# Kernel optimization log

Measured on AMD Instinct MI355X. Metric: run time of the kernel, lower is better.

## Reference

```python
import jax, jax.numpy as jnp
import numpy as np

M_DIM, Z_DIM, C = 256, 128, 32
N, L = 512, 384


def setup_inputs() -> dict:
    key = jax.random.key(0)
    ks = jax.random.split(key, 9)
    s = 1.0 / np.sqrt(M_DIM)
    return {
        "m": jax.random.normal(ks[0], (N, L, M_DIM), dtype=jnp.float32),
        "ln_gamma": jnp.ones((M_DIM,), jnp.float32),
        "ln_beta": jnp.zeros((M_DIM,), jnp.float32),
        "w1": jax.random.normal(ks[1], (M_DIM, C), jnp.float32) * s,
        "b1": jnp.zeros((C,), jnp.float32),
        "w2": jax.random.normal(ks[2], (M_DIM, C), jnp.float32) * s,
        "b2": jnp.zeros((C,), jnp.float32),
        "w3": jax.random.normal(ks[3], (C * C, Z_DIM), jnp.float32) * (1.0 / np.sqrt(C * C)),
        "b3": jnp.zeros((Z_DIM,), jnp.float32),
    }


def _layernorm(x, gamma, beta, eps=1e-5):
    mu = jnp.mean(x, axis=-1, keepdims=True)
    var = jnp.mean(jnp.square(x - mu), axis=-1, keepdims=True)
    return (x - mu) * jax.lax.rsqrt(var + eps) * gamma + beta


def reference(m, ln_gamma, ln_beta, w1, b1, w2, b2, w3, b3):
    n = m.shape[0]
    o = _layernorm(m, ln_gamma, ln_beta)          # (N, L, D)
    a = o @ w2 + b2                                # (N, L, C)  linear2
    b = o @ w1 + b1                                # (N, L, C)  linear1
    # mean over N of outer products: reassociated as a single contraction over n
    op = jnp.einsum('nia,njb->ijab', a, b) / n     # (L, L, C, C)
    ll = op.shape[0]
    z = op.reshape(ll, ll, -1) @ w3 + b3           # (L, L, Z)
    return z
```

## Files before the change

kernel.cpp:

```cpp
#include <hip/hip_runtime.h>
#include <hip/hip_bf16.h>
#include <stdint.h>

#define L_DIM 384
#define MD    256
#define CC    32
#define ZD    128
#define NB    512
#define K2    1024
#define MROWS 12288

typedef __attribute__((ext_vector_type(4))) float  f32x4;
typedef __attribute__((ext_vector_type(8))) short  bf16x8;

typedef __attribute__((address_space(1))) unsigned char* gcp;
typedef __attribute__((address_space(3))) unsigned char* lcp;

#define SBAR()  __builtin_amdgcn_s_barrier()
#define LGKM0() asm volatile("s_waitcnt lgkmcnt(0)" ::: "memory")
#define VMW(n)  asm volatile("s_waitcnt vmcnt(" #n ")" ::: "memory")
#define PRIO1() __builtin_amdgcn_s_setprio(1)
#define PRIO0() __builtin_amdgcn_s_setprio(0)

__device__ __forceinline__ unsigned short f2bf(float x) {
    union { float f; unsigned u; } v; v.f = x;
    unsigned r = v.u + 0x7fffu + ((v.u >> 16) & 1u);
    return (unsigned short)(r >> 16);
}

__device__ __forceinline__ uint2 pack4(unsigned short a, unsigned short b,
                                       unsigned short c, unsigned short d) {
    uint2 r; r.x = (unsigned)a | ((unsigned)b << 16);
    r.y = (unsigned)c | ((unsigned)d << 16); return r;
}

__global__ __launch_bounds__(256) void prep_kernel(
    const float* __restrict__ w1, const float* __restrict__ w2,
    const float* __restrict__ w3,
    unsigned short* __restrict__ w3frag, unsigned short* __restrict__ wfrag)
{
    int idx = blockIdx.x * 256 + threadIdx.x;
    if (idx < 131072) {
        int e = idx & 7, lane = (idx >> 3) & 63, zg = (idx >> 9) & 7, ks = idx >> 12;
        int k2p = ks * 32 + ((lane >> 4) << 3) + e;
        int wrow = (k2p & 31) * 32 + (k2p >> 5);
        int z  = zg * 16 + (lane & 15);
        w3frag[idx] = f2bf(w3[(size_t)wrow * ZD + z]);
    } else {
        int j = idx - 131072;
        int e = j & 7, lane = (j >> 3) & 63, nf = (j >> 9) & 3, ks = j >> 11;
        int c = nf * 16 + (lane & 15);
        int d = ks * 32 + ((lane >> 4) << 3) + e;
        float v = (c < CC) ? w2[d * CC + c] : w1[d * CC + (c - CC)];
        wfrag[j] = f2bf(v);
    }
}

__global__ __launch_bounds__(256, 4) void ln_proj_kernel(
    const float* __restrict__ mm, const float* __restrict__ gamma, const float* __restrict__ beta,
    const unsigned short* __restrict__ wfrag,
    const float* __restrict__ b1, const float* __restrict__ b2,
    unsigned short* __restrict__ At, unsigned short* __restrict__ Bt)
{
    __shared__ alignas(16) char o_b[32768];

    const int tid = threadIdx.x, wv = tid >> 6, lane = tid & 63;
    const int l0 = blockIdx.y * 2;
    const int n0 = blockIdx.x * 32;

    const int l_loc = wv >> 1;
    const int nbase = (wv & 1) << 4;
    const int l_g = l0 + l_loc;
    f32x4 g4 = *(const f32x4*)(gamma + lane * 4);
    f32x4 e4 = *(const f32x4*)(beta + lane * 4);

    #pragma unroll 4
    for (int r = 0; r < 16; ++r) {
        int row_loc = wv * 16 + r;
        int n_g = n0 + nbase + r;
        const float* src = mm + ((size_t)n_g * L_DIM + l_g) * MD + lane * 4;
        f32x4 x = *(const f32x4*)src;
        float s  = x[0] + x[1] + x[2] + x[3];
        float s2 = x[0]*x[0] + x[1]*x[1] + x[2]*x[2] + x[3]*x[3];
        #pragma unroll
        for (int off = 32; off > 0; off >>= 1) {
            s  += __shfl_xor(s,  off);
            s2 += __shfl_xor(s2, off);
        }
        float mu  = s * (1.0f / MD);
        float var = s2 * (1.0f / MD) - mu * mu;
        float rs  = rsqrtf(var + 1e-5f);
        unsigned short o0 = f2bf((x[0] - mu) * rs * g4[0] + e4[0]);
        unsigned short o1 = f2bf((x[1] - mu) * rs * g4[1] + e4[1]);
        unsigned short o2 = f2bf((x[2] - mu) * rs * g4[2] + e4[2]);
        unsigned short o3 = f2bf((x[3] - mu) * rs * g4[3] + e4[3]);
        *(uint2*)(o_b + row_loc * 512 + ((lane * 8) ^ ((row_loc & 7) << 4))) = pack4(o0, o1, o2, o3);
    }

    f32x4 acc[4] = {{0,0,0,0},{0,0,0,0},{0,0,0,0},{0,0,0,0}};
    const int lrow = lane & 15;
    const int kq16 = (lane >> 4) << 4;
    const int arow = wv * 16 + lrow;
    #pragma unroll
    for (int ks = 0; ks < 8; ++ks) {
        bf16x8 a = *(const bf16x8*)(o_b + arow * 512 + ((ks * 64 + kq16) ^ ((arow & 7) << 4)));
        #pragma unroll
        for (int nf = 0; nf < 4; ++nf) {
            bf16x8 b = *(const bf16x8*)(wfrag + (size_t)((ks * 4 + nf) * 64 + lane) * 8);
            acc[nf] = __builtin_amdgcn_mfma_f32_16x16x32_bf16(a, b, acc[nf], 0, 0, 0);
        }
    }

    const int rr0 = wv * 16 + ((lane >> 4) << 2);
    const int n_gw = n0 + (rr0 & 31);
    const int l_gw = l0 + (rr0 >> 5);
    #pragma unroll
    for (int nf = 0; nf < 4; ++nf) {
        int c = nf * 16 + lrow;
        float bias = (c < CC) ? b2[c] : b1[c - CC];
        unsigned short ob0 = f2bf(acc[nf][0] + bias);
        unsigned short ob1 = f2bf(acc[nf][1] + bias);
        unsigned short ob2 = f2bf(acc[nf][2] + bias);
        unsigned short ob3 = f2bf(acc[nf][3] + bias);
        unsigned short* dst = ((c < CC) ? At : Bt) + (size_t)(l_gw * CC + (c & 31)) * NB + n_gw;
        *(uint2*)dst = pack4(ob0, ob1, ob2, ob3);
    }
}

__global__ __launch_bounds__(512, 2) void opm_kernel(
    const unsigned short* __restrict__ At, const unsigned short* __restrict__ Bt,
    const unsigned short* __restrict__ w3frag, const float* __restrict__ b3,
    float* __restrict__ Z)
{
    __shared__ alignas(128) char smem[131072];
    char* const Ab = smem;
    char* const Bb = smem + 65536;

    const int tid = threadIdx.x, wv = tid >> 6, lane = tid & 63;

    const int lin = blockIdx.y * 48 + blockIdx.x;
    const int xcd = lin & 7, chunk = lin >> 3;
    const int i0 = (xcd * 6 + (chunk % 6)) * 256;
    const int j0 = (chunk / 6) * 256;

    const int lrow = lane & 15;
    const int kq16 = (lane >> 4) << 4;
    const int wr = (wv >> 2) * 128, wc = (wv & 3) * 64;

    auto stage = [&](const unsigned short* __restrict__ src, int tile0, int kt,
                     int half, int isA) {
        #pragma unroll
        for (int q = 0; q < 2; ++q) {
            int rl0 = q * 64 + wv * 8;
            int rl  = rl0 + (lane >> 3);
            int rc  = isA ? ((rl  & 63) + ((rl  >> 6) << 7) + half * 64)
                          : ((rl  & 31) + ((rl  >> 5) << 6) + half * 32);
            int rc0 = isA ? ((rl0 & 63) + ((rl0 >> 6) << 7) + half * 64)
                          : ((rl0 & 31) + ((rl0 >> 5) << 6) + half * 32);
            const unsigned short* g = src + (size_t)(tile0 + rc) * NB + kt * 64
                                      + (((lane & 7) ^ (lane >> 3)) << 3);
            char* l = (isA ? Ab : Bb) + (kt & 1) * 32768 + rc0 * 128;
            __builtin_amdgcn_global_load_lds((gcp)g, (lcp)l, 16, 0, 0);
        }
    };

    f32x4 acc[8][4] = {};
    bf16x8 av[8], bl[4], bh[4];

    auto rdA = [&](const char* ab, int qrow) {
        #pragma unroll
        for (int mfl = 0; mfl < 4; ++mfl) {
            int row = wr + qrow * 64 + mfl * 16 + lrow;
            const char* p = ab + row * 128;
            av[mfl*2+0] = *(const bf16x8*)(p + ((     kq16) ^ ((row & 7) << 4)));
            av[mfl*2+1] = *(const bf16x8*)(p + ((64 + kq16) ^ ((row & 7) << 4)));
        }
    };
    auto rdB = [&](const char* bb, int qcol, bf16x8* bv) {
        #pragma unroll
        for (int nfl = 0; nfl < 2; ++nfl) {
            int col = wc + qcol * 32 + nfl * 16 + lrow;
            const char* p = bb + col * 128;
            bv[nfl*2+0] = *(const bf16x8*)(p + ((     kq16) ^ ((col & 7) << 4)));
            bv[nfl*2+1] = *(const bf16x8*)(p + ((64 + kq16) ^ ((col & 7) << 4)));
        }
    };
    auto MM = [&](bf16x8* bv, int mbase, int nbase) {
        #pragma unroll
        for (int mfl = 0; mfl < 4; ++mfl)
            #pragma unroll
            for (int nfl = 0; nfl < 2; ++nfl)
                #pragma unroll
                for (int ks = 0; ks < 2; ++ks)
                    acc[mbase+mfl][nbase+nfl] = __builtin_amdgcn_mfma_f32_16x16x32_bf16(
                        av[mfl*2+ks], bv[nfl*2+ks], acc[mbase+mfl][nbase+nfl], 0, 0, 0);
    };

    stage(At, i0, 0, 0, 1); stage(At, i0, 0, 1, 1);
    stage(Bt, j0, 0, 0, 0); stage(Bt, j0, 0, 1, 0);
    stage(At, i0, 1, 0, 1); stage(At, i0, 1, 1, 1);
    stage(Bt, j0, 1, 0, 0); stage(Bt, j0, 1, 1, 0);
    VMW(8);
    SBAR();

    const char* a0 = Ab;           const char* b0 = Bb;
    const char* a1 = Ab + 32768;   const char* b1 = Bb + 32768;

    for (int t = 0; t < 3; ++t) {
        const int ktc = 2*t + 2, ktd = 2*t + 3;
        rdA(a0, 0); rdB(b0, 0, bl);
        SBAR(); LGKM0(); PRIO1(); MM(bl, 0, 0); PRIO0(); SBAR();
        rdB(b0, 1, bh); stage(At, i0, ktc, 0, 1);
        SBAR(); LGKM0(); PRIO1(); MM(bh, 0, 2); PRIO0(); SBAR();
        rdA(a0, 1); stage(Bt, j0, ktc, 0, 0);
        SBAR(); LGKM0(); PRIO1(); MM(bh, 4, 2); PRIO0(); SBAR();
        stage(Bt, j0, ktc, 1, 0);
        SBAR(); LGKM0(); PRIO1(); MM(bl, 4, 0); PRIO0(); VMW(6); SBAR();
        rdA(a1, 0); rdB(b1, 0, bl); stage(At, i0, ktc, 1, 1);
        SBAR(); LGKM0(); PRIO1(); MM(bl, 0, 0); PRIO0(); SBAR();
        rdB(b1, 1, bh); stage(At, i0, ktd, 0, 1);
        SBAR(); LGKM0(); PRIO1(); MM(bh, 0, 2); PRIO0(); SBAR();
        rdA(a1, 1); stage(Bt, j0, ktd, 0, 0);
        SBAR(); LGKM0(); PRIO1(); MM(bh, 4, 2); PRIO0(); SBAR();
        stage(Bt, j0, ktd, 1, 0); stage(At, i0, ktd, 1, 1);
        SBAR(); LGKM0(); PRIO1(); MM(bl, 4, 0); PRIO0(); VMW(8); SBAR();
    }

    rdA(a0, 0); rdB(b0, 0, bl);
    SBAR(); LGKM0(); PRIO1(); MM(bl, 0, 0); PRIO0(); SBAR();
    rdB(b0, 1, bh);
    SBAR(); LGKM0(); PRIO1(); MM(bh, 0, 2); PRIO0(); SBAR();
    rdA(a0, 1);
    SBAR(); LGKM0(); PRIO1(); MM(bh, 4, 2); PRIO0(); SBAR();
    SBAR(); LGKM0(); PRIO1(); MM(bl, 4, 0); PRIO0(); VMW(0); SBAR();
    rdA(a1, 0); rdB(b1, 0, bl);
    SBAR(); LGKM0(); PRIO1(); MM(bl, 0, 0); PRIO0(); SBAR();
    rdB(b1, 1, bh);
    SBAR(); LGKM0(); PRIO1(); MM(bh, 0, 2); PRIO0(); SBAR();
    rdA(a1, 1);
    SBAR(); LGKM0(); PRIO1(); MM(bh, 4, 2); PRIO0(); SBAR();
    SBAR(); LGKM0(); PRIO1(); MM(bl, 4, 0); PRIO0(); SBAR();

    char* const opb = smem;
    const int pfb = (wv >> 2) * 2, zgb = (wv & 3) * 2;
    const int row0 = pfb * 16 + lrow, row1 = row0 + 16;
    const int lq = lane >> 4;

    auto ldW = [&](int ks, int zg) -> bf16x8 {
        return *(const bf16x8*)(w3frag + (size_t)((ks * 8 + zg) * 64 + lane) * 8);
    };
    auto ldP = [&](int row, int ks) -> bf16x8 {
        int g = ks * 4 + lq;
        int b = g >> 2, jj = g & 3;
        int inner = (b * 64 + jj * 16) ^ (((b >> 1) & 7) << 4) ^ ((row & 7) << 4);
        return *(const bf16x8*)(opb + row * 2048 + inner);
    };

    bf16x8 wA0 = ldW(0, zgb), wA1 = ldW(0, zgb + 1);
    bf16x8 wB0 = ldW(1, zgb), wB1 = ldW(1, zgb + 1);

    const float scale = 1.0f / (float)NB;
    #pragma unroll
    for (int mf = 0; mf < 8; ++mf) {
        #pragma unroll
        for (int nf = 0; nf < 4; ++nf) {
            int col = wc + nf * 16 + lrow;
            int b = col & 31;
            int row = wr + mf * 16 + ((lane >> 4) << 2);
            int pl = ((row >> 5) << 3) | (col >> 5);
            int a0e = row & 31;
            int inner = (b * 64 + a0e * 2) ^ (((b >> 1) & 7) << 4) ^ ((pl & 7) << 4);
            *(uint2*)(opb + pl * 2048 + inner) =
                pack4(f2bf(acc[mf][nf][0] * scale), f2bf(acc[mf][nf][1] * scale),
                      f2bf(acc[mf][nf][2] * scale), f2bf(acc[mf][nf][3] * scale));
        }
    }
    __syncthreads();

    f32x4 acc2[2][2] = {};
    bf16x8 pA0 = ldP(row0, 0), pA1 = ldP(row1, 0);
    bf16x8 pB0 = ldP(row0, 1), pB1 = ldP(row1, 1);
    for (int ks = 0; ks < 32; ks += 2) {
        bf16x8 wN0 = {}, wN1 = {}, pN0 = {}, pN1 = {};
        bf16x8 wM0 = {}, wM1 = {}, pM0 = {}, pM1 = {};
        if (ks + 2 < 32) {
            wN0 = ldW(ks + 2, zgb); wN1 = ldW(ks + 2, zgb + 1);
            pN0 = ldP(row0, ks + 2); pN1 = ldP(row1, ks + 2);
            wM0 = ldW(ks + 3, zgb); wM1 = ldW(ks + 3, zgb + 1);
            pM0 = ldP(row0, ks + 3); pM1 = ldP(row1, ks + 3);
        }
        PRIO1();
        acc2[0][0] = __builtin_amdgcn_mfma_f32_16x16x32_bf16(pA0, wA0, acc2[0][0], 0, 0, 0);
        acc2[0][1] = __builtin_amdgcn_mfma_f32_16x16x32_bf16(pA0, wA1, acc2[0][1], 0, 0, 0);
        acc2[1][0] = __builtin_amdgcn_mfma_f32_16x16x32_bf16(pA1, wA0, acc2[1][0], 0, 0, 0);
        acc2[1][1] = __builtin_amdgcn_mfma_f32_16x16x32_bf16(pA1, wA1, acc2[1][1], 0, 0, 0);
        acc2[0][0] = __builtin_amdgcn_mfma_f32_16x16x32_bf16(pB0, wB0, acc2[0][0], 0, 0, 0);
        acc2[0][1] = __builtin_amdgcn_mfma_f32_16x16x32_bf16(pB0, wB1, acc2[0][1], 0, 0, 0);
        acc2[1][0] = __builtin_amdgcn_mfma_f32_16x16x32_bf16(pB1, wB0, acc2[1][0], 0, 0, 0);
        acc2[1][1] = __builtin_amdgcn_mfma_f32_16x16x32_bf16(pB1, wB1, acc2[1][1], 0, 0, 0);
        PRIO0();
        wA0 = wN0; wA1 = wN1; pA0 = pN0; pA1 = pN1;
        wB0 = wM0; wB1 = wM1; pB0 = pM0; pB1 = pM1;
    }

    const int pq = (lane >> 4) << 2;
    #pragma unroll
    for (int p = 0; p < 2; ++p) {
        #pragma unroll
        for (int zi = 0; zi < 2; ++zi) {
            int zc = (zgb + zi) * 16 + lrow;
            float bias = b3[zc];
            #pragma unroll
            for (int rr = 0; rr < 4; ++rr) {
                int pl = (pfb + p) * 16 + pq + rr;
                int ii = (i0 >> 5) + (pl >> 3);
                int jj = (j0 >> 5) + (pl & 7);
                Z[((size_t)ii * L_DIM + jj) * ZD + zc] = acc2[p][zi][rr] + bias;
            }
        }
    }
}

extern "C" void kernel_launch(void* const* d_in, const int* in_sizes, int n_in,
                              void* d_out, int out_size, void* d_ws, size_t ws_size,
                              hipStream_t stream)
{
    const float* mm    = (const float*)d_in[0];
    const float* gamma = (const float*)d_in[1];
    const float* beta  = (const float*)d_in[2];
    const float* w1    = (const float*)d_in[3];
    const float* b1    = (const float*)d_in[4];
    const float* w2    = (const float*)d_in[5];
    const float* b2    = (const float*)d_in[6];
    const float* w3    = (const float*)d_in[7];
    const float* b3    = (const float*)d_in[8];

    unsigned short* At     = (unsigned short*)d_ws;
    unsigned short* Bt     = At + (size_t)MROWS * NB;
    unsigned short* w3frag = Bt + (size_t)MROWS * NB;
    unsigned short* wfrag  = w3frag + 131072;

    prep_kernel<<<576, 256, 0, stream>>>(w1, w2, w3, w3frag, wfrag);
    ln_proj_kernel<<<dim3(16, 192), 256, 0, stream>>>(mm, gamma, beta, wfrag, b1, b2, At, Bt);
    opm_kernel<<<dim3(48, 48), 512, 0, stream>>>(At, Bt, w3frag, b3, (float*)d_out);
}
```

Baseline: 258.2 us.

## Switch main GEMM to 32x32x16 MFMA with restaged software pipeline

Replaces the 16x16x32 MFMA tiling of the per-block 256x256 outer-product GEMM with 32x32x16 MFMAs, accumulating into 4x2 f32x16 tiles per wave. LDS fragment reads are restructured to match, which changes how much data is reused per MFMA and how many LDS reads are issued. The global-to-LDS staging schedule is reorganized into fewer, larger phases with different vmcnt waits, and the epilogue that writes bf16 outer products to LDS is rewritten for the new accumulator layout. The larger MFMA shape should cut LDS traffic per flop, but the new pipeline depth and barrier placement could expose more memory latency.

```diff
diff --git a/kernel.cpp b/kernel.cpp
--- a/kernel.cpp
+++ b/kernel.cpp
@@ -10,8 +10,9 @@
 #define K2    1024
 #define MROWS 12288
 
-typedef __attribute__((ext_vector_type(4))) float  f32x4;
-typedef __attribute__((ext_vector_type(8))) short  bf16x8;
+typedef __attribute__((ext_vector_type(4)))  float f32x4;
+typedef __attribute__((ext_vector_type(16))) float f32x16;
+typedef __attribute__((ext_vector_type(8)))  short bf16x8;
 
 typedef __attribute__((address_space(1))) unsigned char* gcp;
 typedef __attribute__((address_space(3))) unsigned char* lcp;
@@ -143,8 +144,9 @@
     const int i0 = (xcd * 6 + (chunk % 6)) * 256;
     const int j0 = (chunk / 6) * 256;
 
-    const int lrow = lane & 15;
-    const int kq16 = (lane >> 4) << 4;
+    const int mrow = lane & 31;
+    const int kb16 = (lane >> 5) << 4;
+    const int swz  = (mrow & 7) << 4;
     const int wr = (wv >> 2) * 128, wc = (wv & 3) * 64;
 
     auto stage = [&](const unsigned short* __restrict__ src, int tile0, int kt,
@@ -164,84 +166,77 @@
         }
     };
 
-    f32x4 acc[8][4] = {};
-    bf16x8 av[8], bl[4], bh[4];
-
-    auto rdA = [&](const char* ab, int qrow) {
-        #pragma unroll
-        for (int mfl = 0; mfl < 4; ++mfl) {
-            int row = wr + qrow * 64 + mfl * 16 + lrow;
-            const char* p = ab + row * 128;
-            av[mfl*2+0] = *(const bf16x8*)(p + ((     kq16) ^ ((row & 7) << 4)));
-            av[mfl*2+1] = *(const bf16x8*)(p + ((64 + kq16) ^ ((row & 7) << 4)));
-        }
-    };
-    auto rdB = [&](const char* bb, int qcol, bf16x8* bv) {
-        #pragma unroll
-        for (int nfl = 0; nfl < 2; ++nfl) {
-            int col = wc + qcol * 32 + nfl * 16 + lrow;
-            const char* p = bb + col * 128;
-            bv[nfl*2+0] = *(const bf16x8*)(p + ((     kq16) ^ ((col & 7) << 4)));
-            bv[nfl*2+1] = *(const bf16x8*)(p + ((64 + kq16) ^ ((col & 7) << 4)));
-        }
-    };
-    auto MM = [&](bf16x8* bv, int mbase, int nbase) {
-        #pragma unroll
-        for (int mfl = 0; mfl < 4; ++mfl)
-            #pragma unroll
-            for (int nfl = 0; nfl < 2; ++nfl)
+    f32x16 acc[4][2] = {};
+    bf16x8 av[2][4], bv[2][4];
+
+    auto rdA32 = [&](const char* ab, int mhalf) {
+        #pragma unroll
+        for (int mfl = 0; mfl < 2; ++mfl) {
+            const char* p = ab + (wr + (mhalf * 2 + mfl) * 32 + mrow) * 128;
+            #pragma unroll
+            for (int ks = 0; ks < 4; ++ks)
+                av[mfl][ks] = *(const bf16x8*)(p + ((ks * 32 + kb16) ^ swz));
+        }
+    };
+    auto rdB32 = [&](const char* bb) {
+        #pragma unroll
+        for (int nf = 0; nf < 2; ++nf) {
+            const char* p = bb + (wc + nf * 32 + mrow) * 128;
+            #pragma unroll
+            for (int ks = 0; ks < 4; ++ks)
+                bv[nf][ks] = *(const bf16x8*)(p + ((ks * 32 + kb16) ^ swz));
+        }
+    };
+    auto MM32 = [&](int mhalf) {
+        #pragma unroll
+        for (int mfl = 0; mfl < 2; ++mfl)
+            #pragma unroll
+            for (int nf = 0; nf < 2; ++nf)
                 #pragma unroll
-                for (int ks = 0; ks < 2; ++ks)
-                    acc[mbase+mfl][nbase+nfl] = __builtin_amdgcn_mfma_f32_16x16x32_bf16(
-                        av[mfl*2+ks], bv[nfl*2+ks], acc[mbase+mfl][nbase+nfl], 0, 0, 0);
-    };
-
-    stage(At, i0, 0, 0, 1); stage(At, i0, 0, 1, 1);
-    stage(Bt, j0, 0, 0, 0); stage(Bt, j0, 0, 1, 0);
-    stage(At, i0, 1, 0, 1); stage(At, i0, 1, 1, 1);
-    stage(Bt, j0, 1, 0, 0); stage(Bt, j0, 1, 1, 0);
-    VMW(8);
+                for (int ks = 0; ks < 4; ++ks)
+                    acc[mhalf * 2 + mfl][nf] = __builtin_amdgcn_mfma_f32_32x32x16_bf16(
+                        av[mfl][ks], bv[nf][ks], acc[mhalf * 2 + mfl][nf], 0, 0, 0);
+    };
+
+    stage(At, i0, 0, 0, 1); stage(Bt, j0, 0, 0, 0);
+    stage(At, i0, 0, 1, 1); stage(Bt, j0, 0, 1, 0);
+    stage(At, i0, 1, 0, 1); stage(Bt, j0, 1, 0, 0);
+    VMW(4);
     SBAR();
 
     const char* a0 = Ab;           const char* b0 = Bb;
     const char* a1 = Ab + 32768;   const char* b1 = Bb + 32768;
 
+    #pragma unroll
     for (int t = 0; t < 3; ++t) {
-        const int ktc = 2*t + 2, ktd = 2*t + 3;
-        rdA(a0, 0); rdB(b0, 0, bl);
-        SBAR(); LGKM0(); PRIO1(); MM(bl, 0, 0); PRIO0(); SBAR();
-        rdB(b0, 1, bh); stage(At, i0, ktc, 0, 1);
-        SBAR(); LGKM0(); PRIO1(); MM(bh, 0, 2); PRIO0(); SBAR();
-        rdA(a0, 1); stage(Bt, j0, ktc, 0, 0);
-        SBAR(); LGKM0(); PRIO1(); MM(bh, 4, 2); PRIO0(); SBAR();
-        stage(Bt, j0, ktc, 1, 0);
-        SBAR(); LGKM0(); PRIO1(); MM(bl, 4, 0); PRIO0(); VMW(6); SBAR();
-        rdA(a1, 0); rdB(b1, 0, bl); stage(At, i0, ktc, 1, 1);
-        SBAR(); LGKM0(); PRIO1(); MM(bl, 0, 0); PRIO0(); SBAR();
-        rdB(b1, 1, bh); stage(At, i0, ktd, 0, 1);
-        SBAR(); LGKM0(); PRIO1(); MM(bh, 0, 2); PRIO0(); SBAR();
-        rdA(a1, 1); stage(Bt, j0, ktd, 0, 0);
-        SBAR(); LGKM0(); PRIO1(); MM(bh, 4, 2); PRIO0(); SBAR();
-        stage(Bt, j0, ktd, 1, 0); stage(At, i0, ktd, 1, 1);
-        SBAR(); LGKM0(); PRIO1(); MM(bl, 4, 0); PRIO0(); VMW(8); SBAR();
-    }
-
-    rdA(a0, 0); rdB(b0, 0, bl);
-    SBAR(); LGKM0(); PRIO1(); MM(bl, 0, 0); PRIO0(); SBAR();
-    rdB(b0, 1, bh);
-    SBAR(); LGKM0(); PRIO1(); MM(bh, 0, 2); PRIO0(); SBAR();
-    rdA(a0, 1);
-    SBAR(); LGKM0(); PRIO1(); MM(bh, 4, 2); PRIO0(); SBAR();
-    SBAR(); LGKM0(); PRIO1(); MM(bl, 4, 0); PRIO0(); VMW(0); SBAR();
-    rdA(a1, 0); rdB(b1, 0, bl);
-    SBAR(); LGKM0(); PRIO1(); MM(bl, 0, 0); PRIO0(); SBAR();
-    rdB(b1, 1, bh);
-    SBAR(); LGKM0(); PRIO1(); MM(bh, 0, 2); PRIO0(); SBAR();
-    rdA(a1, 1);
-    SBAR(); LGKM0(); PRIO1(); MM(bh, 4, 2); PRIO0(); SBAR();
-    SBAR(); LGKM0(); PRIO1(); MM(bl, 4, 0); PRIO0(); SBAR();
+        rdA32(a0, 0); rdB32(b0);
+        stage(At, i0, 2*t + 1, 1, 1); stage(Bt, j0, 2*t + 1, 1, 0);
+        SBAR(); LGKM0(); PRIO1(); MM32(0); PRIO0(); SBAR();
+        rdA32(a0, 1);
+        stage(At, i0, 2*t + 2, 0, 1); stage(Bt, j0, 2*t + 2, 0, 0);
+        SBAR(); LGKM0(); PRIO1(); MM32(1); PRIO0(); VMW(4); SBAR();
+        rdA32(a1, 0); rdB32(b1);
+        stage(At, i0, 2*t + 2, 1, 1); stage(Bt, j0, 2*t + 2, 1, 0);
+        SBAR(); LGKM0(); PRIO1(); MM32(0); PRIO0(); SBAR();
+        rdA32(a1, 1);
+        stage(At, i0, 2*t + 3, 0, 1); stage(Bt, j0, 2*t + 3, 0, 0);
+        SBAR(); LGKM0(); PRIO1(); MM32(1); PRIO0(); VMW(4); SBAR();
+    }
+
+    rdA32(a0, 0); rdB32(b0);
+    stage(At, i0, 7, 1, 1); stage(Bt, j0, 7, 1, 0);
+    SBAR(); LGKM0(); PRIO1(); MM32(0); PRIO0(); SBAR();
+    rdA32(a0, 1);
+    SBAR(); LGKM0(); PRIO1(); MM32(1); PRIO0(); VMW(0); SBAR();
+    rdA32(a1, 0); rdB32(b1);
+    MM32(0);
+    rdA32(a1, 1);
+    MM32(1);
+    __syncthreads();
 
     char* const opb = smem;
+    const int lrow = lane & 15;
+    const int kq16 = (lane >> 4) << 4;
     const int pfb = (wv >> 2) * 2, zgb = (wv & 3) * 2;
     const int row0 = pfb * 16 + lrow, row1 = row0 + 16;
     const int lq = lane >> 4;
@@ -260,19 +255,23 @@
     bf16x8 wB0 = ldW(1, zgb), wB1 = ldW(1, zgb + 1);
 
     const float scale = 1.0f / (float)NB;
-    #pragma unroll
-    for (int mf = 0; mf < 8; ++mf) {
-        #pragma unroll
-        for (int nf = 0; nf < 4; ++nf) {
-            int col = wc + nf * 16 + lrow;
-            int b = col & 31;
-            int row = wr + mf * 16 + ((lane >> 4) << 2);
-            int pl = ((row >> 5) << 3) | (col >> 5);
-            int a0e = row & 31;
-            int inner = (b * 64 + a0e * 2) ^ (((b >> 1) & 7) << 4) ^ ((pl & 7) << 4);
-            *(uint2*)(opb + pl * 2048 + inner) =
-                pack4(f2bf(acc[mf][nf][0] * scale), f2bf(acc[mf][nf][1] * scale),
-                      f2bf(acc[mf][nf][2] * scale), f2bf(acc[mf][nf][3] * scale));
+    const int bcol = lane & 31;
+    const int hq4  = (lane >> 5) << 2;
+    #pragma unroll
+    for (int mf = 0; mf < 4; ++mf) {
+        #pragma unroll
+        for (int nf = 0; nf < 2; ++nf) {
+            int j_loc = ((wc >> 5) + nf);
+            int pl = (((wr >> 5) + mf) << 3) | j_loc;
+            int swp = (((bcol >> 1) & 7) << 4) ^ ((pl & 7) << 4);
+            #pragma unroll
+            for (int q = 0; q < 4; ++q) {
+                int a0e = q * 8 + hq4;
+                int inner = (bcol * 64 + a0e * 2) ^ swp;
+                *(uint2*)(opb + pl * 2048 + inner) =
+                    pack4(f2bf(acc[mf][nf][4*q+0] * scale), f2bf(acc[mf][nf][4*q+1] * scale),
+                          f2bf(acc[mf][nf][4*q+2] * scale), f2bf(acc[mf][nf][4*q+3] * scale));
+            }
         }
     }
     __syncthreads();
```

After: 259.0 us. About the same (+0.3%).

## Store B operand in MFMA fragment layout and load it directly to registers

Applied to the files above, without the earlier changes.

The projection kernel now writes the B operand (linear1 output) pre-swizzled into MFMA fragment order, so the outer-product kernel loads B straight from global memory into registers instead of staging it through LDS. The main loop is simplified to a double-buffered A-only LDS pipeline with per-iteration register prefetch of B and far fewer barriers. The grid becomes 1-D. This removes the LDS traffic and synchronisation for B, at the cost of B being re-read from global or L2 by every wave and holding more registers for the prefetched fragments.

```diff
diff --git a/kernel.cpp b/kernel.cpp
--- a/kernel.cpp
+++ b/kernel.cpp
@@ -10,8 +10,8 @@
 #define K2    1024
 #define MROWS 12288
 
-typedef __attribute__((ext_vector_type(4))) float  f32x4;
-typedef __attribute__((ext_vector_type(8))) short  bf16x8;
+typedef __attribute__((ext_vector_type(4)))  float f32x4;
+typedef __attribute__((ext_vector_type(8)))  short bf16x8;
 
 typedef __attribute__((address_space(1))) unsigned char* gcp;
 typedef __attribute__((address_space(3))) unsigned char* lcp;
@@ -118,12 +118,17 @@
     for (int nf = 0; nf < 4; ++nf) {
         int c = nf * 16 + lrow;
         float bias = (c < CC) ? b2[c] : b1[c - CC];
-        unsigned short ob0 = f2bf(acc[nf][0] + bias);
-        unsigned short ob1 = f2bf(acc[nf][1] + bias);
-        unsigned short ob2 = f2bf(acc[nf][2] + bias);
-        unsigned short ob3 = f2bf(acc[nf][3] + bias);
-        unsigned short* dst = ((c < CC) ? At : Bt) + (size_t)(l_gw * CC + (c & 31)) * NB + n_gw;
-        *(uint2*)dst = pack4(ob0, ob1, ob2, ob3);
+        uint2 pk = pack4(f2bf(acc[nf][0] + bias), f2bf(acc[nf][1] + bias),
+                         f2bf(acc[nf][2] + bias), f2bf(acc[nf][3] + bias));
+        if (c < CC) {
+            *(uint2*)(At + (size_t)(l_gw * CC + c) * NB + n_gw) = pk;
+        } else {
+            int c31 = c - CC;
+            int f = l_gw * 2 + (c31 >> 4);
+            int lanep = (c31 & 15) + (((n_gw >> 3) & 3) << 4);
+            size_t addr = ((size_t)(f * 16 + (n_gw >> 5)) * 64 + lanep) * 8 + (n_gw & 7);
+            *(uint2*)(Bt + addr) = pk;
+        }
     }
 }
 
@@ -134,11 +139,10 @@
 {
     __shared__ alignas(128) char smem[131072];
     char* const Ab = smem;
-    char* const Bb = smem + 65536;
 
     const int tid = threadIdx.x, wv = tid >> 6, lane = tid & 63;
 
-    const int lin = blockIdx.y * 48 + blockIdx.x;
+    const int lin = blockIdx.x;
     const int xcd = lin & 7, chunk = lin >> 3;
     const int i0 = (xcd * 6 + (chunk % 6)) * 256;
     const int j0 = (chunk / 6) * 256;
@@ -147,99 +151,62 @@
     const int kq16 = (lane >> 4) << 4;
     const int wr = (wv >> 2) * 128, wc = (wv & 3) * 64;
 
-    auto stage = [&](const unsigned short* __restrict__ src, int tile0, int kt,
-                     int half, int isA) {
-        #pragma unroll
-        for (int q = 0; q < 2; ++q) {
-            int rl0 = q * 64 + wv * 8;
-            int rl  = rl0 + (lane >> 3);
-            int rc  = isA ? ((rl  & 63) + ((rl  >> 6) << 7) + half * 64)
-                          : ((rl  & 31) + ((rl  >> 5) << 6) + half * 32);
-            int rc0 = isA ? ((rl0 & 63) + ((rl0 >> 6) << 7) + half * 64)
-                          : ((rl0 & 31) + ((rl0 >> 5) << 6) + half * 32);
-            const unsigned short* g = src + (size_t)(tile0 + rc) * NB + kt * 64
-                                      + (((lane & 7) ^ (lane >> 3)) << 3);
-            char* l = (isA ? Ab : Bb) + (kt & 1) * 32768 + rc0 * 128;
-            __builtin_amdgcn_global_load_lds((gcp)g, (lcp)l, 16, 0, 0);
+    const int srow = lane >> 3;
+    const int spre = ((lane & 7) ^ srow) << 3;
+
+    auto stageA = [&](int t) {
+        char* base = Ab + (t & 1) * 32768;
+        #pragma unroll
+        for (int g = 0; g < 4; ++g) {
+            int rl0 = g * 64 + wv * 8;
+            const unsigned short* gp = At + (size_t)(i0 + rl0 + srow) * NB + t * 64 + spre;
+            __builtin_amdgcn_global_load_lds((gcp)gp, (lcp)(base + rl0 * 128), 16, 0, 0);
         }
     };
 
+    const int fb0 = (j0 + wc) >> 4;
+    auto loadB = [&](bf16x8* bv, int t) {
+        #pragma unroll
+        for (int nf = 0; nf < 4; ++nf)
+            #pragma unroll
+            for (int kk = 0; kk < 2; ++kk)
+                bv[nf * 2 + kk] = *(const bf16x8*)(Bt +
+                    (size_t)((fb0 + nf) * 16 + (t * 2 + kk)) * 512 + lane * 8);
+    };
+
     f32x4 acc[8][4] = {};
-    bf16x8 av[8], bl[4], bh[4];
-
-    auto rdA = [&](const char* ab, int qrow) {
-        #pragma unroll
-        for (int mfl = 0; mfl < 4; ++mfl) {
-            int row = wr + qrow * 64 + mfl * 16 + lrow;
-            const char* p = ab + row * 128;
-            av[mfl*2+0] = *(const bf16x8*)(p + ((     kq16) ^ ((row & 7) << 4)));
-            av[mfl*2+1] = *(const bf16x8*)(p + ((64 + kq16) ^ ((row & 7) << 4)));
-        }
-    };
-    auto rdB = [&](const char* bb, int qcol, bf16x8* bv) {
-        #pragma unroll
-        for (int nfl = 0; nfl < 2; ++nfl) {
-            int col = wc + qcol * 32 + nfl * 16 + lrow;
-            const char* p = bb + col * 128;
-            bv[nfl*2+0] = *(const bf16x8*)(p + ((     kq16) ^ ((col & 7) << 4)));
-            bv[nfl*2+1] = *(const bf16x8*)(p + ((64 + kq16) ^ ((col & 7) << 4)));
-        }
-    };
-    auto MM = [&](bf16x8* bv, int mbase, int nbase) {
-        #pragma unroll
-        for (int mfl = 0; mfl < 4; ++mfl)
+    bf16x8 bcur[8], bnxt[8], av[8];
+
+    stageA(0); loadB(bcur, 0); stageA(1);
+    VMW(12);
+    SBAR();
+
+    #pragma unroll
+    for (int t = 0; t < 8; ++t) {
+        if (t < 7) { stageA(t + 1); loadB(bnxt, t + 1); }
+        const char* ab = Ab + (t & 1) * 32768;
+        #pragma unroll
+        for (int kk = 0; kk < 2; ++kk) {
             #pragma unroll
-            for (int nfl = 0; nfl < 2; ++nfl)
+            for (int mf = 0; mf < 8; ++mf) {
+                int row = wr + mf * 16 + lrow;
+                av[mf] = *(const bf16x8*)(ab + row * 128 + ((kk * 64 + kq16) ^ ((row & 7) << 4)));
+            }
+            LGKM0();
+            PRIO1();
+            #pragma unroll
+            for (int mf = 0; mf < 8; ++mf)
                 #pragma unroll
-                for (int ks = 0; ks < 2; ++ks)
-                    acc[mbase+mfl][nbase+nfl] = __builtin_amdgcn_mfma_f32_16x16x32_bf16(
-                        av[mfl*2+ks], bv[nfl*2+ks], acc[mbase+mfl][nbase+nfl], 0, 0, 0);
-    };
-
-    stage(At, i0, 0, 0, 1); stage(At, i0, 0, 1, 1);
-    stage(Bt, j0, 0, 0, 0); stage(Bt, j0, 0, 1, 0);
-    stage(At, i0, 1, 0, 1); stage(At, i0, 1, 1, 1);
-    stage(Bt, j0, 1, 0, 0); stage(Bt, j0, 1, 1, 0);
-    VMW(8);
-    SBAR();
-
-    const char* a0 = Ab;           const char* b0 = Bb;
-    const char* a1 = Ab + 32768;   const char* b1 = Bb + 32768;
-
-    for (int t = 0; t < 3; ++t) {
-        const int ktc = 2*t + 2, ktd = 2*t + 3;
-        rdA(a0, 0); rdB(b0, 0, bl);
-        SBAR(); LGKM0(); PRIO1(); MM(bl, 0, 0); PRIO0(); SBAR();
-        rdB(b0, 1, bh); stage(At, i0, ktc, 0, 1);
-        SBAR(); LGKM0(); PRIO1(); MM(bh, 0, 2); PRIO0(); SBAR();
-        rdA(a0, 1); stage(Bt, j0, ktc, 0, 0);
-        SBAR(); LGKM0(); PRIO1(); MM(bh, 4, 2); PRIO0(); SBAR();
-        stage(Bt, j0, ktc, 1, 0);
-        SBAR(); LGKM0(); PRIO1(); MM(bl, 4, 0); PRIO0(); VMW(6); SBAR();
-        rdA(a1, 0); rdB(b1, 0, bl); stage(At, i0, ktc, 1, 1);
-        SBAR(); LGKM0(); PRIO1(); MM(bl, 0, 0); PRIO0(); SBAR();
-        rdB(b1, 1, bh); stage(At, i0, ktd, 0, 1);
-        SBAR(); LGKM0(); PRIO1(); MM(bh, 0, 2); PRIO0(); SBAR();
-        rdA(a1, 1); stage(Bt, j0, ktd, 0, 0);
-        SBAR(); LGKM0(); PRIO1(); MM(bh, 4, 2); PRIO0(); SBAR();
-        stage(Bt, j0, ktd, 1, 0); stage(At, i0, ktd, 1, 1);
-        SBAR(); LGKM0(); PRIO1(); MM(bl, 4, 0); PRIO0(); VMW(8); SBAR();
-    }
-
-    rdA(a0, 0); rdB(b0, 0, bl);
-    SBAR(); LGKM0(); PRIO1(); MM(bl, 0, 0); PRIO0(); SBAR();
-    rdB(b0, 1, bh);
-    SBAR(); LGKM0(); PRIO1(); MM(bh, 0, 2); PRIO0(); SBAR();
-    rdA(a0, 1);
-    SBAR(); LGKM0(); PRIO1(); MM(bh, 4, 2); PRIO0(); SBAR();
-    SBAR(); LGKM0(); PRIO1(); MM(bl, 4, 0); PRIO0(); VMW(0); SBAR();
-    rdA(a1, 0); rdB(b1, 0, bl);
-    SBAR(); LGKM0(); PRIO1(); MM(bl, 0, 0); PRIO0(); SBAR();
-    rdB(b1, 1, bh);
-    SBAR(); LGKM0(); PRIO1(); MM(bh, 0, 2); PRIO0(); SBAR();
-    rdA(a1, 1);
-    SBAR(); LGKM0(); PRIO1(); MM(bh, 4, 2); PRIO0(); SBAR();
-    SBAR(); LGKM0(); PRIO1(); MM(bl, 4, 0); PRIO0(); SBAR();
+                for (int nf = 0; nf < 4; ++nf)
+                    acc[mf][nf] = __builtin_amdgcn_mfma_f32_16x16x32_bf16(
+                        av[mf], bcur[nf * 2 + kk], acc[mf][nf], 0, 0, 0);
+            PRIO0();
+        }
+        #pragma unroll
+        for (int q = 0; q < 8; ++q) bcur[q] = bnxt[q];
+        if (t < 7) { VMW(8); SBAR(); }
+    }
+    __syncthreads();
 
     char* const opb = smem;
     const int pfb = (wv >> 2) * 2, zgb = (wv & 3) * 2;
@@ -265,11 +232,11 @@
         #pragma unroll
         for (int nf = 0; nf < 4; ++nf) {
             int col = wc + nf * 16 + lrow;
-            int b = col & 31;
+            int bcol = col & 31;
             int row = wr + mf * 16 + ((lane >> 4) << 2);
             int pl = ((row >> 5) << 3) | (col >> 5);
             int a0e = row & 31;
-            int inner = (b * 64 + a0e * 2) ^ (((b >> 1) & 7) << 4) ^ ((pl & 7) << 4);
+            int inner = (bcol * 64 + a0e * 2) ^ (((bcol >> 1) & 7) << 4) ^ ((pl & 7) << 4);
             *(uint2*)(opb + pl * 2048 + inner) =
                 pack4(f2bf(acc[mf][nf][0] * scale), f2bf(acc[mf][nf][1] * scale),
                       f2bf(acc[mf][nf][2] * scale), f2bf(acc[mf][nf][3] * scale));
@@ -342,5 +309,5 @@
 
     prep_kernel<<<576, 256, 0, stream>>>(w1, w2, w3, w3frag, wfrag);
     ln_proj_kernel<<<dim3(16, 192), 256, 0, stream>>>(mm, gamma, beta, wfrag, b1, b2, At, Bt);
-    opm_kernel<<<dim3(48, 48), 512, 0, stream>>>(At, Bt, w3frag, b3, (float*)d_out);
-}
+    opm_kernel<<<2304, 512, 0, stream>>>(At, Bt, w3frag, b3, (float*)d_out);
+}
```

New measurement: 256.5 us. Within noise of the previous version (-0.7%).
